# Optimization experiments

Hardware: AMD Instinct MI355X
Metric: run time of the kernel (lower is better)

## Reference

```python
import jax, jax.numpy as jnp
import numpy as np

B, S, NQ, FFN, EMB = 8, 4096, 8, 2048, 512


def setup_inputs() -> dict:
    key = jax.random.key(0)
    k0, k1, k2, k3 = jax.random.split(key, 4)
    x = jax.random.normal(k0, (B, S, NQ), dtype=jnp.float32)
    theta = jax.random.normal(k1, (NQ,), dtype=jnp.float32)  # trainable RY angles
    W1 = jax.random.normal(k2, (NQ, FFN), dtype=jnp.float32) / np.float32(np.sqrt(NQ))
    b1 = jnp.zeros((FFN,), dtype=jnp.float32)
    W2 = jax.random.normal(k3, (FFN, EMB), dtype=jnp.float32) / np.float32(np.sqrt(FFN))
    b2 = jnp.zeros((EMB,), dtype=jnp.float32)
    return {"x": x, "theta": theta, "W1": W1, "b1": b1, "W2": W2, "b2": b2}


def reference(x, theta, W1, b1, W2, b2):
    # Quantum layer: per wire i, state RY(theta_i) RX(x_i) |0>; no entangling gates,
    # so the state is a product state and <PauliZ_i> = cos(x_i) * cos(theta_i) exactly.
    # This fuses the per-token / per-gate simulation loop into one batched expression.
    q = jnp.cos(x) * jnp.cos(theta)                     # [B, S, NQ]
    # Dropout is identity at eval time.
    h = jax.nn.relu(jnp.einsum("bsq,qf->bsf", q, W1) + b1)  # [B, S, FFN]
    out = jnp.einsum("bsf,fe->bse", h, W2) + b2             # [B, S, EMB]
    return out
```

## Files before the change

kernel.cpp:

```cpp
#include <hip/hip_runtime.h>

#define T_TOK 32768
#define NQ    8
#define FFN   2048
#define EMB   512
#define BM    128
#define BN    128
#define BK    64
#define NCHUNK (FFN / BK)
#define HPAD  72

typedef __attribute__((ext_vector_type(8))) short  short8;
typedef __attribute__((ext_vector_type(4))) float  float4v;

__device__ __forceinline__ unsigned short f2bf(float f) {
  unsigned int u = __float_as_uint(f);
  u += 0x7fffu + ((u >> 16) & 1u);
  return (unsigned short)(u >> 16);
}

__device__ __forceinline__ unsigned pk2bf(float lo, float hi) {
#if __has_builtin(__builtin_amdgcn_cvt_pk_bf16_f32)
  typedef __attribute__((ext_vector_type(2))) __bf16 bf2;
  bf2 p = __builtin_amdgcn_cvt_pk_bf16_f32(lo, hi);
  return *(unsigned*)&p;
#else
  return (unsigned)f2bf(lo) | ((unsigned)f2bf(hi) << 16);
#endif
}

__global__ void prep_all(const float* __restrict__ W1,
                         const float* __restrict__ W2,
                         unsigned short* __restrict__ w1t,
                         unsigned short* __restrict__ w2t) {
  __shared__ float t[32][33];
  const int kb = blockIdx.x * 32;
  const int nb = blockIdx.y * 32;
  const int c = threadIdx.x & 31, r0 = threadIdx.x >> 5;
#pragma unroll
  for (int p = 0; p < 4; ++p) {
    int r = r0 + p * 8;
    t[r][c] = W2[(size_t)(kb + r) * EMB + nb + c];
  }
  __syncthreads();
#pragma unroll
  for (int p = 0; p < 4; ++p) {
    int r = r0 + p * 8;
    w2t[(size_t)(nb + r) * FFN + kb + c] = f2bf(t[c][r]);
  }
  if (blockIdx.x == 0) {
    const int base = blockIdx.y * 1024 + threadIdx.x * 4;
#pragma unroll
    for (int e = 0; e < 4; ++e) {
      int idx = base + e;
      int f = idx >> 3, i = idx & 7;
      w1t[idx] = f2bf(W1[i * FFN + f]);
    }
  }
}

__global__ __launch_bounds__(256, 2) void ffq_main(
    const float* __restrict__ x,
    const float* __restrict__ theta,
    const unsigned short* __restrict__ w1t,
    const float* __restrict__ b1,
    const unsigned short* __restrict__ w2t,
    const float* __restrict__ b2,
    float* __restrict__ out) {

  __shared__ unsigned short h_lds[BM][HPAD];
  __shared__ unsigned short w2_lds[BN * BK];
  __shared__ unsigned short w1_lds[FFN * NQ];
  __shared__ float          b1_lds[FFN];

  const int tid  = threadIdx.x;
  const int wave = tid >> 6;
  const int lane = tid & 63;
  const int l15  = lane & 15;
  const int quad = lane >> 4;
  const int tok0 = blockIdx.x * BM;
  const int n0   = blockIdx.y * BN;
  const int wr   = wave >> 1;
  const int wc   = wave & 1;

#pragma unroll
  for (int i = 0; i < 8; ++i) {
    const unsigned short* g = w1t + i * 2048 + tid * 8;
    unsigned short* l = w1_lds + i * 2048 + tid * 8;
    __builtin_amdgcn_global_load_lds(
        (const __attribute__((address_space(1))) void*)g,
        (__attribute__((address_space(3))) void*)l, 16, 0, 0);
  }
#pragma unroll
  for (int i = 0; i < 2; ++i) {
    const float* g = b1 + i * 1024 + tid * 4;
    float* l = b1_lds + i * 1024 + tid * 4;
    __builtin_amdgcn_global_load_lds(
        (const __attribute__((address_space(1))) void*)g,
        (__attribute__((address_space(3))) void*)l, 16, 0, 0);
  }

  float cth[8];
  {
    const float4* tp = (const float4*)theta;
    float4 t0 = tp[0], t1 = tp[1];
    cth[0] = __cosf(t0.x); cth[1] = __cosf(t0.y);
    cth[2] = __cosf(t0.z); cth[3] = __cosf(t0.w);
    cth[4] = __cosf(t1.x); cth[5] = __cosf(t1.y);
    cth[6] = __cosf(t1.z); cth[7] = __cosf(t1.w);
  }
  short8 bq[2];
#pragma unroll
  for (int g = 0; g < 2; ++g) {
    short8 v = (short8){0,0,0,0,0,0,0,0};
    if (lane < 16) {
      int tok = tok0 + 32 * wave + 16 * g + lane;
      const float4* xp = (const float4*)(x + (size_t)tok * NQ);
      float4 x0 = xp[0], x1 = xp[1];
      float q0 = __cosf(x0.x) * cth[0], q1 = __cosf(x0.y) * cth[1];
      float q2 = __cosf(x0.z) * cth[2], q3 = __cosf(x0.w) * cth[3];
      float q4 = __cosf(x1.x) * cth[4], q5 = __cosf(x1.y) * cth[5];
      float q6 = __cosf(x1.z) * cth[6], q7 = __cosf(x1.w) * cth[7];
      uint4 uu;
      uu.x = pk2bf(q0, q1); uu.y = pk2bf(q2, q3);
      uu.z = pk2bf(q4, q5); uu.w = pk2bf(q6, q7);
      v = *(short8*)&uu;
    }
    bq[g] = v;
  }

  float4v acc[4][4];
#pragma unroll
  for (int i = 0; i < 4; ++i)
#pragma unroll
    for (int j = 0; j < 4; ++j)
      acc[i][j] = (float4v){0.f, 0.f, 0.f, 0.f};

  for (int kc = 0; kc < NCHUNK; ++kc) {
    const int k0 = kc * BK;

    __syncthreads();

    {
      const int r = tid >> 3;
      const int c = tid & 7;
#pragma unroll
      for (int issue = 0; issue < 4; ++issue) {
        const int row    = issue * 32 + r;
        const int gchunk = c ^ (row & 7);
        const unsigned short* g =
            w2t + (size_t)(n0 + row) * FFN + k0 + gchunk * 8;
        unsigned short* l = &w2_lds[issue * 2048 + tid * 8];
        __builtin_amdgcn_global_load_lds(
            (const __attribute__((address_space(1))) void*)g,
            (__attribute__((address_space(3))) void*)l, 16, 0, 0);
      }
    }

#pragma unroll
    for (int kt = 0; kt < 4; ++kt) {
      short8 aw = (short8){0,0,0,0,0,0,0,0};
      if (lane < 16)
        aw = *(const short8*)&w1_lds[(k0 + kt * 16 + l15) * NQ];
      float4 bias = *(const float4*)&b1_lds[k0 + kt * 16 + quad * 4];
      float4v c0 = (float4v){0.f, 0.f, 0.f, 0.f};
      float4v c1 = (float4v){0.f, 0.f, 0.f, 0.f};
      c0 = __builtin_amdgcn_mfma_f32_16x16x32_bf16(aw, bq[0], c0, 0, 0, 0);
      c1 = __builtin_amdgcn_mfma_f32_16x16x32_bf16(aw, bq[1], c1, 0, 0, 0);
      float v0[4], v1[4];
#pragma unroll
      for (int r = 0; r < 4; ++r) {
        float a0 = c0[r] + bias[r]; v0[r] = a0 > 0.f ? a0 : 0.f;
        float a1 = c1[r] + bias[r]; v1[r] = a1 > 0.f ? a1 : 0.f;
      }
      uint2 p0, p1;
      p0.x = pk2bf(v0[0], v0[1]); p0.y = pk2bf(v0[2], v0[3]);
      p1.x = pk2bf(v1[0], v1[1]); p1.y = pk2bf(v1[2], v1[3]);
      *((uint2*)&h_lds[32 * wave + l15][kt * 16 + quad * 4])      = p0;
      *((uint2*)&h_lds[32 * wave + 16 + l15][kt * 16 + quad * 4]) = p1;
    }

    __syncthreads();

#pragma unroll
    for (int ks = 0; ks < 2; ++ks) {
      short8 af[4], bf[4];
#pragma unroll
      for (int mt = 0; mt < 4; ++mt)
        af[mt] = *(const short8*)&h_lds[wr * 64 + mt * 16 + l15]
                                       [ks * 32 + quad * 8];
#pragma unroll
      for (int nt = 0; nt < 4; ++nt) {
        const int n  = wc * 64 + nt * 16 + l15;
        const int sc = (ks * 4 + quad) ^ (n & 7);
        bf[nt] = *(const short8*)&w2_lds[n * BK + sc * 8];
      }
#pragma unroll
      for (int mt = 0; mt < 4; ++mt)
#pragma unroll
        for (int nt = 0; nt < 4; ++nt)
          acc[mt][nt] = __builtin_amdgcn_mfma_f32_16x16x32_bf16(
              af[mt], bf[nt], acc[mt][nt], 0, 0, 0);
    }
  }

#pragma unroll
  for (int nt = 0; nt < 4; ++nt) {
    const int col = n0 + wc * 64 + nt * 16 + l15;
    const float bv = b2[col];
#pragma unroll
    for (int mt = 0; mt < 4; ++mt) {
      const int row0 = tok0 + wr * 64 + mt * 16 + quad * 4;
#pragma unroll
      for (int r = 0; r < 4; ++r) {
        out[(size_t)(row0 + r) * EMB + col] = acc[mt][nt][r] + bv;
      }
    }
  }
}

extern "C" void kernel_launch(void* const* d_in, const int* in_sizes, int n_in,
                              void* d_out, int out_size, void* d_ws, size_t ws_size,
                              hipStream_t stream) {
  const float* x     = (const float*)d_in[0];
  const float* theta = (const float*)d_in[1];
  const float* W1    = (const float*)d_in[2];
  const float* b1    = (const float*)d_in[3];
  const float* W2    = (const float*)d_in[4];
  const float* b2    = (const float*)d_in[5];
  float* out = (float*)d_out;

  unsigned short* w1t = (unsigned short*)d_ws;
  unsigned short* w2t = w1t + FFN * NQ;

  prep_all<<<dim3(FFN / 32, EMB / 32), 256, 0, stream>>>(W1, W2, w1t, w2t);

  dim3 grid(T_TOK / BM, EMB / BN);
  ffq_main<<<grid, 256, 0, stream>>>(x, theta, w1t, b1, w2t, b2, out);
}
```

Measured before the change: 187.7 us.

## Double-buffer W2 and hidden tiles, doubling the token tile to 256

Doubles the token tile to 256 rows and runs 512 threads (8 waves) per block. Both the hidden-activation tile and the W2 tile are double-buffered in LDS. The next chunk's W2 async load and first-layer MFMA are issued alongside the current chunk's second GEMM, which removes one barrier per chunk and overlaps load with compute. The trade-off is about 146KB of LDS per block, so only one block fits per CU. The grid also shrinks to 512 blocks on 256 CUs, which may cost latency hiding and cause tail imbalance.

```diff
diff --git a/kernel.cpp b/kernel.cpp
--- a/kernel.cpp
+++ b/kernel.cpp
@@ -4,7 +4,7 @@
 #define NQ    8
 #define FFN   2048
 #define EMB   512
-#define BM    128
+#define BM    256
 #define BN    128
 #define BK    64
 #define NCHUNK (FFN / BK)
@@ -59,7 +59,7 @@
   }
 }
 
-__global__ __launch_bounds__(256, 2) void ffq_main(
+__global__ __launch_bounds__(512, 2) void ffq_main(
     const float* __restrict__ x,
     const float* __restrict__ theta,
     const unsigned short* __restrict__ w1t,
@@ -68,8 +68,8 @@
     const float* __restrict__ b2,
     float* __restrict__ out) {
 
-  __shared__ unsigned short h_lds[BM][HPAD];
-  __shared__ unsigned short w2_lds[BN * BK];
+  __shared__ unsigned short h_lds[2][BM][HPAD];
+  __shared__ unsigned short w2_lds[2][BN * BK];
   __shared__ unsigned short w1_lds[FFN * NQ];
   __shared__ float          b1_lds[FFN];
 
@@ -84,17 +84,16 @@
   const int wc   = wave & 1;
 
 #pragma unroll
-  for (int i = 0; i < 8; ++i) {
-    const unsigned short* g = w1t + i * 2048 + tid * 8;
-    unsigned short* l = w1_lds + i * 2048 + tid * 8;
+  for (int i = 0; i < 4; ++i) {
+    const unsigned short* g = w1t + i * 4096 + tid * 8;
+    unsigned short* l = w1_lds + i * 4096 + tid * 8;
     __builtin_amdgcn_global_load_lds(
         (const __attribute__((address_space(1))) void*)g,
         (__attribute__((address_space(3))) void*)l, 16, 0, 0);
   }
-#pragma unroll
-  for (int i = 0; i < 2; ++i) {
-    const float* g = b1 + i * 1024 + tid * 4;
-    float* l = b1_lds + i * 1024 + tid * 4;
+  {
+    const float* g = b1 + tid * 4;
+    float* l = b1_lds + tid * 4;
     __builtin_amdgcn_global_load_lds(
         (const __attribute__((address_space(1))) void*)g,
         (__attribute__((address_space(3))) void*)l, 16, 0, 0);
@@ -129,39 +128,27 @@
     bq[g] = v;
   }
 
-  float4v acc[4][4];
-#pragma unroll
-  for (int i = 0; i < 4; ++i)
-#pragma unroll
-    for (int j = 0; j < 4; ++j)
-      acc[i][j] = (float4v){0.f, 0.f, 0.f, 0.f};
-
-  for (int kc = 0; kc < NCHUNK; ++kc) {
+  auto stage_w2 = [&](int kc, int buf) {
+    const int r = tid >> 3;
+    const int c = tid & 7;
+#pragma unroll
+    for (int issue = 0; issue < 2; ++issue) {
+      const int row    = issue * 64 + r;
+      const int gchunk = c ^ (row & 7);
+      const unsigned short* g =
+          w2t + (size_t)(n0 + row) * FFN + kc * BK + gchunk * 8;
+      unsigned short* l = &w2_lds[buf][issue * 4096 + tid * 8];
+      __builtin_amdgcn_global_load_lds(
+          (const __attribute__((address_space(1))) void*)g,
+          (__attribute__((address_space(3))) void*)l, 16, 0, 0);
+    }
+  };
+
+  auto gemm1 = [&](int kc, int buf) {
     const int k0 = kc * BK;
-
-    __syncthreads();
-
-    {
-      const int r = tid >> 3;
-      const int c = tid & 7;
-#pragma unroll
-      for (int issue = 0; issue < 4; ++issue) {
-        const int row    = issue * 32 + r;
-        const int gchunk = c ^ (row & 7);
-        const unsigned short* g =
-            w2t + (size_t)(n0 + row) * FFN + k0 + gchunk * 8;
-        unsigned short* l = &w2_lds[issue * 2048 + tid * 8];
-        __builtin_amdgcn_global_load_lds(
-            (const __attribute__((address_space(1))) void*)g,
-            (__attribute__((address_space(3))) void*)l, 16, 0, 0);
-      }
-    }
-
 #pragma unroll
     for (int kt = 0; kt < 4; ++kt) {
-      short8 aw = (short8){0,0,0,0,0,0,0,0};
-      if (lane < 16)
-        aw = *(const short8*)&w1_lds[(k0 + kt * 16 + l15) * NQ];
+      short8 aw = *(const short8*)&w1_lds[(k0 + kt * 16 + l15) * NQ];
       float4 bias = *(const float4*)&b1_lds[k0 + kt * 16 + quad * 4];
       float4v c0 = (float4v){0.f, 0.f, 0.f, 0.f};
       float4v c1 = (float4v){0.f, 0.f, 0.f, 0.f};
@@ -176,24 +163,41 @@
       uint2 p0, p1;
       p0.x = pk2bf(v0[0], v0[1]); p0.y = pk2bf(v0[2], v0[3]);
       p1.x = pk2bf(v1[0], v1[1]); p1.y = pk2bf(v1[2], v1[3]);
-      *((uint2*)&h_lds[32 * wave + l15][kt * 16 + quad * 4])      = p0;
-      *((uint2*)&h_lds[32 * wave + 16 + l15][kt * 16 + quad * 4]) = p1;
-    }
+      *((uint2*)&h_lds[buf][32 * wave + l15][kt * 16 + quad * 4])      = p0;
+      *((uint2*)&h_lds[buf][32 * wave + 16 + l15][kt * 16 + quad * 4]) = p1;
+    }
+  };
+
+  float4v acc[4][4];
+#pragma unroll
+  for (int i = 0; i < 4; ++i)
+#pragma unroll
+    for (int j = 0; j < 4; ++j)
+      acc[i][j] = (float4v){0.f, 0.f, 0.f, 0.f};
+
+  stage_w2(0, 0);
+  __syncthreads();
+  gemm1(0, 0);
+
+  for (int kc = 0; kc < NCHUNK; ++kc) {
+    const int p = kc & 1;
 
     __syncthreads();
+
+    if (kc + 1 < NCHUNK) stage_w2(kc + 1, p ^ 1);
 
 #pragma unroll
     for (int ks = 0; ks < 2; ++ks) {
       short8 af[4], bf[4];
 #pragma unroll
       for (int mt = 0; mt < 4; ++mt)
-        af[mt] = *(const short8*)&h_lds[wr * 64 + mt * 16 + l15]
-                                       [ks * 32 + quad * 8];
+        af[mt] = *(const short8*)&h_lds[p][wr * 64 + mt * 16 + l15]
+                                          [ks * 32 + quad * 8];
 #pragma unroll
       for (int nt = 0; nt < 4; ++nt) {
         const int n  = wc * 64 + nt * 16 + l15;
         const int sc = (ks * 4 + quad) ^ (n & 7);
-        bf[nt] = *(const short8*)&w2_lds[n * BK + sc * 8];
+        bf[nt] = *(const short8*)&w2_lds[p][n * BK + sc * 8];
       }
 #pragma unroll
       for (int mt = 0; mt < 4; ++mt)
@@ -202,6 +206,8 @@
           acc[mt][nt] = __builtin_amdgcn_mfma_f32_16x16x32_bf16(
               af[mt], bf[nt], acc[mt][nt], 0, 0, 0);
     }
+
+    if (kc + 1 < NCHUNK) gemm1(kc + 1, p ^ 1);
   }
 
 #pragma unroll
@@ -236,5 +242,5 @@
   prep_all<<<dim3(FFN / 32, EMB / 32), 256, 0, stream>>>(W1, W2, w1t, w2t);
 
   dim3 grid(T_TOK / BM, EMB / BN);
-  ffq_main<<<grid, 256, 0, stream>>>(x, theta, w1t, b1, w2t, b2, out);
-}
+  ffq_main<<<grid, 512, 0, stream>>>(x, theta, w1t, b1, w2t, b2, out);
+}
```

Result: slower. 193.9 us (+3.3%).

## Keep hidden activations in registers and feed second GEMM directly from MFMA output

Applied to the files above, without the earlier changes.

Replaces the LDS round-trip for the ReLU hidden tile with a register-resident chain. Each wave computes its own 16x16 hidden fragments with 16x16x16 bf16 MFMAs, with the bias folded into the accumulator. Those fragments are reused directly as A operands for the second GEMM, and W2 fragments are read straight from global memory instead of being staged in LDS. This removes the per-chunk barriers and the LDS traffic, and raises occupancy to 4 blocks. In exchange, the first GEMM is recomputed redundantly across the two column waves, and every W2 access becomes a small uncoalesced 8-byte global load that relies on L2/L1 hits.

```diff
diff --git a/kernel.cpp b/kernel.cpp
--- a/kernel.cpp
+++ b/kernel.cpp
@@ -6,11 +6,10 @@
 #define EMB   512
 #define BM    128
 #define BN    128
-#define BK    64
-#define NCHUNK (FFN / BK)
-#define HPAD  72
+#define KSTEP 16
+#define NKU   (FFN / KSTEP)
 
-typedef __attribute__((ext_vector_type(8))) short  short8;
+typedef __attribute__((ext_vector_type(4))) short  short4v;
 typedef __attribute__((ext_vector_type(4))) float  float4v;
 
 __device__ __forceinline__ unsigned short f2bf(float f) {
@@ -59,7 +58,7 @@
   }
 }
 
-__global__ __launch_bounds__(256, 2) void ffq_main(
+__global__ __launch_bounds__(256, 4) void ffq_main(
     const float* __restrict__ x,
     const float* __restrict__ theta,
     const unsigned short* __restrict__ w1t,
@@ -68,8 +67,6 @@
     const float* __restrict__ b2,
     float* __restrict__ out) {
 
-  __shared__ unsigned short h_lds[BM][HPAD];
-  __shared__ unsigned short w2_lds[BN * BK];
   __shared__ unsigned short w1_lds[FFN * NQ];
   __shared__ float          b1_lds[FFN];
 
@@ -100,34 +97,28 @@
         (__attribute__((address_space(3))) void*)l, 16, 0, 0);
   }
 
-  float cth[8];
-  {
-    const float4* tp = (const float4*)theta;
-    float4 t0 = tp[0], t1 = tp[1];
-    cth[0] = __cosf(t0.x); cth[1] = __cosf(t0.y);
-    cth[2] = __cosf(t0.z); cth[3] = __cosf(t0.w);
-    cth[4] = __cosf(t1.x); cth[5] = __cosf(t1.y);
-    cth[6] = __cosf(t1.z); cth[7] = __cosf(t1.w);
+  short4v bq[4];
+#pragma unroll
+  for (int mt = 0; mt < 4; ++mt) bq[mt] = (short4v){0, 0, 0, 0};
+  if (quad < 2) {
+    const float4 th = *(const float4*)(theta + quad * 4);
+    const float c0 = __cosf(th.x), c1 = __cosf(th.y);
+    const float c2 = __cosf(th.z), c3 = __cosf(th.w);
+#pragma unroll
+    for (int mt = 0; mt < 4; ++mt) {
+      const int tok = tok0 + wr * 64 + mt * 16 + l15;
+      const float4 xv = *(const float4*)(x + (size_t)tok * NQ + quad * 4);
+      uint2 p;
+      p.x = pk2bf(__cosf(xv.x) * c0, __cosf(xv.y) * c1);
+      p.y = pk2bf(__cosf(xv.z) * c2, __cosf(xv.w) * c3);
+      bq[mt] = *(short4v*)&p;
+    }
   }
-  short8 bq[2];
+
+  const unsigned short* w2p[4];
 #pragma unroll
-  for (int g = 0; g < 2; ++g) {
-    short8 v = (short8){0,0,0,0,0,0,0,0};
-    if (lane < 16) {
-      int tok = tok0 + 32 * wave + 16 * g + lane;
-      const float4* xp = (const float4*)(x + (size_t)tok * NQ);
-      float4 x0 = xp[0], x1 = xp[1];
-      float q0 = __cosf(x0.x) * cth[0], q1 = __cosf(x0.y) * cth[1];
-      float q2 = __cosf(x0.z) * cth[2], q3 = __cosf(x0.w) * cth[3];
-      float q4 = __cosf(x1.x) * cth[4], q5 = __cosf(x1.y) * cth[5];
-      float q6 = __cosf(x1.z) * cth[6], q7 = __cosf(x1.w) * cth[7];
-      uint4 uu;
-      uu.x = pk2bf(q0, q1); uu.y = pk2bf(q2, q3);
-      uu.z = pk2bf(q4, q5); uu.w = pk2bf(q6, q7);
-      v = *(short8*)&uu;
-    }
-    bq[g] = v;
-  }
+  for (int nt = 0; nt < 4; ++nt)
+    w2p[nt] = w2t + (size_t)(n0 + wc * 64 + nt * 16 + l15) * FFN + quad * 4;
 
   float4v acc[4][4];
 #pragma unroll
@@ -136,72 +127,40 @@
     for (int j = 0; j < 4; ++j)
       acc[i][j] = (float4v){0.f, 0.f, 0.f, 0.f};
 
-  for (int kc = 0; kc < NCHUNK; ++kc) {
-    const int k0 = kc * BK;
+  __syncthreads();
 
-    __syncthreads();
+#pragma unroll 2
+  for (int ku = 0; ku < NKU; ++ku) {
+    short4v b2f[4];
+#pragma unroll
+    for (int nt = 0; nt < 4; ++nt)
+      b2f[nt] = *(const short4v*)(w2p[nt] + ku * KSTEP);
 
-    {
-      const int r = tid >> 3;
-      const int c = tid & 7;
+    const int awoff = ((ku * 16 + l15) * 8 + quad * 4) & 16383;
+    short4v aw = *(const short4v*)&w1_lds[awoff];
+    float4v bias = *(const float4v*)&b1_lds[ku * 16 + quad * 4];
+
+    short4v a2[4];
 #pragma unroll
-      for (int issue = 0; issue < 4; ++issue) {
-        const int row    = issue * 32 + r;
-        const int gchunk = c ^ (row & 7);
-        const unsigned short* g =
-            w2t + (size_t)(n0 + row) * FFN + k0 + gchunk * 8;
-        unsigned short* l = &w2_lds[issue * 2048 + tid * 8];
-        __builtin_amdgcn_global_load_lds(
-            (const __attribute__((address_space(1))) void*)g,
-            (__attribute__((address_space(3))) void*)l, 16, 0, 0);
-      }
+    for (int mt = 0; mt < 4; ++mt) {
+      float4v c1 = __builtin_amdgcn_mfma_f32_16x16x16bf16_1k(
+          aw, bq[mt], bias, 0, 0, 0);
+      float v0 = c1[0] > 0.f ? c1[0] : 0.f;
+      float v1 = c1[1] > 0.f ? c1[1] : 0.f;
+      float v2 = c1[2] > 0.f ? c1[2] : 0.f;
+      float v3 = c1[3] > 0.f ? c1[3] : 0.f;
+      uint2 p;
+      p.x = pk2bf(v0, v1);
+      p.y = pk2bf(v2, v3);
+      a2[mt] = *(short4v*)&p;
     }
 
 #pragma unroll
-    for (int kt = 0; kt < 4; ++kt) {
-      short8 aw = (short8){0,0,0,0,0,0,0,0};
-      if (lane < 16)
-        aw = *(const short8*)&w1_lds[(k0 + kt * 16 + l15) * NQ];
-      float4 bias = *(const float4*)&b1_lds[k0 + kt * 16 + quad * 4];
-      float4v c0 = (float4v){0.f, 0.f, 0.f, 0.f};
-      float4v c1 = (float4v){0.f, 0.f, 0.f, 0.f};
-      c0 = __builtin_amdgcn_mfma_f32_16x16x32_bf16(aw, bq[0], c0, 0, 0, 0);
-      c1 = __builtin_amdgcn_mfma_f32_16x16x32_bf16(aw, bq[1], c1, 0, 0, 0);
-      float v0[4], v1[4];
+    for (int mt = 0; mt < 4; ++mt)
 #pragma unroll
-      for (int r = 0; r < 4; ++r) {
-        float a0 = c0[r] + bias[r]; v0[r] = a0 > 0.f ? a0 : 0.f;
-        float a1 = c1[r] + bias[r]; v1[r] = a1 > 0.f ? a1 : 0.f;
-      }
-      uint2 p0, p1;
-      p0.x = pk2bf(v0[0], v0[1]); p0.y = pk2bf(v0[2], v0[3]);
-      p1.x = pk2bf(v1[0], v1[1]); p1.y = pk2bf(v1[2], v1[3]);
-      *((uint2*)&h_lds[32 * wave + l15][kt * 16 + quad * 4])      = p0;
-      *((uint2*)&h_lds[32 * wave + 16 + l15][kt * 16 + quad * 4]) = p1;
-    }
-
-    __syncthreads();
-
-#pragma unroll
-    for (int ks = 0; ks < 2; ++ks) {
-      short8 af[4], bf[4];
-#pragma unroll
-      for (int mt = 0; mt < 4; ++mt)
-        af[mt] = *(const short8*)&h_lds[wr * 64 + mt * 16 + l15]
-                                       [ks * 32 + quad * 8];
-#pragma unroll
-      for (int nt = 0; nt < 4; ++nt) {
-        const int n  = wc * 64 + nt * 16 + l15;
-        const int sc = (ks * 4 + quad) ^ (n & 7);
-        bf[nt] = *(const short8*)&w2_lds[n * BK + sc * 8];
-      }
-#pragma unroll
-      for (int mt = 0; mt < 4; ++mt)
-#pragma unroll
-        for (int nt = 0; nt < 4; ++nt)
-          acc[mt][nt] = __builtin_amdgcn_mfma_f32_16x16x32_bf16(
-              af[mt], bf[nt], acc[mt][nt], 0, 0, 0);
-    }
+      for (int nt = 0; nt < 4; ++nt)
+        acc[mt][nt] = __builtin_amdgcn_mfma_f32_16x16x16bf16_1k(
+            a2[mt], b2f[nt], acc[mt][nt], 0, 0, 0);
   }
 
 #pragma unroll
```

After: 312.5 us. 66.5% more time.
